# Kernel tuning notes

Measured on AMD Instinct MI355X. Metric: run time of the kernel, lower is better.

Reference implementation:

```python
import jax, jax.numpy as jnp
import numpy as np

DIM = 1024
HEADS = 16
HEAD_DIM = DIM // HEADS
HIDDEN = int(DIM * 4.0)
EPS = 1e-5


def setup_inputs() -> dict:
    key = jax.random.key(0)
    ks = jax.random.split(key, 16)
    s = 0.02
    inp = {
        'x': jax.random.normal(ks[0], (2, 2048, DIM), dtype=jnp.float32),
        'g1': jnp.ones((DIM,), jnp.float32),
        'b1': jnp.zeros((DIM,), jnp.float32),
        'Wq': jax.random.normal(ks[1], (DIM, DIM)) * s,
        'bq': jnp.zeros((DIM,), jnp.float32),
        'Wk': jax.random.normal(ks[2], (DIM, DIM)) * s,
        'bk': jnp.zeros((DIM,), jnp.float32),
        'Wv': jax.random.normal(ks[3], (DIM, DIM)) * s,
        'bv': jnp.zeros((DIM,), jnp.float32),
        'Wo': jax.random.normal(ks[4], (DIM, DIM)) * s,
        'bo': jnp.zeros((DIM,), jnp.float32),
        'g2': jnp.ones((DIM,), jnp.float32),
        'b2': jnp.zeros((DIM,), jnp.float32),
        'W1': jax.random.normal(ks[5], (DIM, HIDDEN)) * s,
        'bf1': jnp.zeros((HIDDEN,), jnp.float32),
        'W2': jax.random.normal(ks[6], (HIDDEN, DIM)) * s,
        'bf2': jnp.zeros((DIM,), jnp.float32),
    }
    return inp


def _layernorm(x, g, b):
    mu = jnp.mean(x, axis=-1, keepdims=True)
    var = jnp.mean((x - mu) ** 2, axis=-1, keepdims=True)
    return (x - mu) * jax.lax.rsqrt(var + EPS) * g + b


def _block(x, g1, b1, Wq, bq, Wk, bk, Wv, bv, Wo, bo, g2, b2, W1, bf1, W2, bf2):
    B, N, C = x.shape
    h = _layernorm(x, g1, b1)
    # project and split heads: [B, H, N, D]
    q = (h @ Wq + bq).reshape(B, N, HEADS, HEAD_DIM).transpose(0, 2, 1, 3)
    k = (h @ Wk + bk).reshape(B, N, HEADS, HEAD_DIM).transpose(0, 2, 1, 3)
    v = (h @ Wv + bv).reshape(B, N, HEADS, HEAD_DIM).transpose(0, 2, 1, 3)
    scale = HEAD_DIM ** -0.5
    attn = jnp.einsum('bhqd,bhkd->bhqk', q, k) * scale
    attn = jax.nn.softmax(attn, axis=-1)
    o = jnp.einsum('bhqk,bhkd->bhqd', attn, v)
    o = o.transpose(0, 2, 1, 3).reshape(B, N, C)
    x = x + (o @ Wo + bo)
    h = _layernorm(x, g2, b2)
    h = jax.nn.gelu(h @ W1 + bf1, approximate=False)
    x = x + (h @ W2 + bf2)
    return x


def reference(x, g1, b1, Wq, bq, Wk, bk, Wv, bv, Wo, bo, g2, b2, W1, bf1, W2, bf2):
    return _block(x, g1, b1, Wq, bq, Wk, bk, Wv, bv, Wo, bo, g2, b2, W1, bf1, W2, bf2)
```

## Files before the change

### kernel.cpp

```cpp
#include <hip/hip_runtime.h>
#include <hip/hip_bf16.h>
#include <math.h>


typedef unsigned short ushort_t;
typedef short short8 __attribute__((ext_vector_type(8)));
typedef float f32x4 __attribute__((ext_vector_type(4)));

#define TOKENS 4096
#define SEQ    2048
#define DIMC   1024
#define HID    4096

__device__ __forceinline__ float bf2f(ushort_t u) {
    union { float f; unsigned int u; } c; c.u = ((unsigned int)u) << 16; return c.f;
}
__device__ __forceinline__ ushort_t f2bf(float f) {
    union { float f; unsigned int u; } c; c.f = f;
    unsigned int u = c.u;
    unsigned int r = u + 0x7fffu + ((u >> 16) & 1u);
    return (ushort_t)(r >> 16);
}
__device__ __forceinline__ float gelu_f(float x) {
    const float y = 0.79788456080286536f * (x + 0.044715f * x * x * x);
    const float t = __expf(-2.0f * fabsf(y));
    const float th = (1.0f - t) / (1.0f + t);
    return 0.5f * x * (1.0f + copysignf(th, y));
}
__device__ __forceinline__ float load_elem(const void* p, size_t i, int isbf) {
    return isbf ? bf2f(((const ushort_t*)p)[i]) : ((const float*)p)[i];
}

__global__ __launch_bounds__(256) void detect_dtype(
    const ushort_t* __restrict__ x, int* __restrict__ flag)
{
    __shared__ int bad;
    if (threadIdx.x == 0) bad = 0;
    __syncthreads();
    for (int i = threadIdx.x; i < 4096; i += 256) {
        float v = bf2f(x[i]);
        if (!(fabsf(v) <= 1e6f)) bad = 1;
    }
    __syncthreads();
    if (threadIdx.x == 0) { flag[0] = (bad == 0) ? 1 : 0; flag[1] = 1; }
}

__global__ __launch_bounds__(256) void transpose_w_all(
    const void* __restrict__ Wq, const void* __restrict__ Wk,
    const void* __restrict__ Wv, const void* __restrict__ Wo,
    const void* __restrict__ W1, const void* __restrict__ W2,
    ushort_t* __restrict__ wsq, ushort_t* __restrict__ w1t,
    ushort_t* __restrict__ w2t, const int* __restrict__ flag)
{
    __shared__ ushort_t tile[32][33];
    const int isbf = *flag;
    const int id = blockIdx.x;
    const void* in; ushort_t* out; int K, N, bx, by;
    if (id < 4096) {
        const int z = id >> 10, t = id & 1023;
        in = z == 0 ? Wq : (z == 1 ? Wk : (z == 2 ? Wv : Wo));
        out = wsq + (size_t)z * DIMC * DIMC;
        K = DIMC; N = DIMC; bx = t & 31; by = t >> 5;
    } else if (id < 8192) {
        const int t = id - 4096;
        in = W1; out = w1t; K = DIMC; N = HID;
        bx = t & 127; by = t >> 7;
    } else {
        const int t = id - 8192;
        in = W2; out = w2t; K = HID; N = DIMC;
        bx = t & 31; by = t >> 5;
    }
    const int kb = by * 32, nb = bx * 32;
    const int tx = threadIdx.x & 31, ty = threadIdx.x >> 5;
    for (int i = 0; i < 4; i++) {
        int k = kb + ty + i * 8;
        tile[ty + i * 8][tx] = f2bf(load_elem(in, (size_t)k * N + nb + tx, isbf));
    }
    __syncthreads();
    for (int i = 0; i < 4; i++) {
        int n = nb + ty + i * 8;
        out[(size_t)n * K + kb + tx] = tile[tx][ty + i * 8];
    }
}

template<int INMODE>
__global__ __launch_bounds__(256) void ln_kernel(
    const void* __restrict__ in, const void* __restrict__ g,
    const void* __restrict__ b, const int* __restrict__ flag,
    ushort_t* __restrict__ out)
{
    const int isbf = *flag;
    const int t = blockIdx.x;
    const int tid = threadIdx.x;
    const size_t base = (size_t)t * DIMC;
    float v[4];
    for (int i = 0; i < 4; i++) {
        int idx = tid + i * 256;
        v[i] = (INMODE == 1) ? ((const float*)in)[base + idx]
                             : load_elem(in, base + idx, isbf);
    }
    float s  = v[0] + v[1] + v[2] + v[3];
    float s2 = v[0]*v[0] + v[1]*v[1] + v[2]*v[2] + v[3]*v[3];
    for (int off = 1; off < 64; off <<= 1) {
        s  += __shfl_xor(s,  off);
        s2 += __shfl_xor(s2, off);
    }
    __shared__ float red[8];
    const int wave = tid >> 6, lane = tid & 63;
    if (lane == 0) { red[wave] = s; red[wave + 4] = s2; }
    __syncthreads();
    s  = red[0] + red[1] + red[2] + red[3];
    s2 = red[4] + red[5] + red[6] + red[7];
    const float mu  = s * (1.0f / DIMC);
    const float var = s2 * (1.0f / DIMC) - mu * mu;
    const float inv = rsqrtf(fmaxf(var, 0.f) + 1e-5f);
    for (int i = 0; i < 4; i++) {
        int idx = tid + i * 256;
        float o = (v[i] - mu) * inv * load_elem(g, idx, isbf) + load_elem(b, idx, isbf);
        out[base + idx] = f2bf(o);
    }
}

template<int BN, int RES, int ACT, int OUTF>
__global__ __launch_bounds__(256) void gemm_bt(
    const ushort_t* __restrict__ A, const ushort_t* __restrict__ BT,
    const void* __restrict__ bias0, const void* __restrict__ bias1,
    const void* __restrict__ bias2, const void* __restrict__ resid,
    void* __restrict__ out0, void* __restrict__ out1, void* __restrict__ out2,
    int M, int N, int K, int Ksub, const int* __restrict__ flag)
{
    constexpr int BM   = 128;
    constexpr int JF   = BN / 32;
    constexpr int ASEG = BM / 16;
    constexpr int SPW  = (BM + BN) / 64;
    __shared__ __align__(16) ushort_t As[3][BM][32];
    __shared__ __align__(16) ushort_t Bs[3][BN][32];
    const int isbf = *flag;
    const int tid = threadIdx.x, lane = tid & 63, wave = tid >> 6;
    const int m0 = blockIdx.y * BM, n0 = blockIdx.x * BN;
    const int wm = (wave & 1) * 64;
    const int wn = (wave >> 1) * (BN / 2);
    const int lm = lane & 15, quad = lane >> 4;

    const void* biasp = bias0;
    void* outp = out0;
    int nout = N;
    int colmask = 0x7fffffff;
    int sel = 0;
    if (OUTF == 3) {
        sel = n0 >> 10;
        biasp = sel == 0 ? bias0 : (sel == 1 ? bias1 : bias2);
        outp  = sel == 0 ? out0  : (sel == 1 ? out1  : out2);
        nout = 1024; colmask = 1023;
    }
    int kbeg = 0;
    if (OUTF == 4) {
        kbeg = blockIdx.z * Ksub;
        outp = blockIdx.z ? out1 : out0;
    }

    f32x4 acc[4][JF];
    for (int i = 0; i < 4; i++)
        for (int j = 0; j < JF; j++)
            acc[i][j] = (f32x4){0.f, 0.f, 0.f, 0.f};

    const int lsw  = lane ^ ((lane >> 3) & 7);
    const int lrow = lsw >> 2;
    const int lcol = (lsw & 3) * 8;
    const int srd  = (4 * lm + quad);
    const int srz  = srd ^ ((srd >> 3) & 7);
    const int rsw  = srz >> 2;
    const int csw  = (srz & 3) * 8;

    const ushort_t* gpp[SPW];
    ushort_t* lpp[3][SPW];
#pragma unroll
    for (int s = 0; s < SPW; s++) {
        const int seg = wave * SPW + s;
        if (seg < ASEG) {
            gpp[s]    = &A[(size_t)(m0 + seg * 16 + lrow) * K + kbeg + lcol];
            lpp[0][s] = &As[0][seg * 16][0];
            lpp[1][s] = &As[1][seg * 16][0];
            lpp[2][s] = &As[2][seg * 16][0];
        } else {
            gpp[s]    = &BT[(size_t)(n0 + (seg - ASEG) * 16 + lrow) * K + kbeg + lcol];
            lpp[0][s] = &Bs[0][(seg - ASEG) * 16][0];
            lpp[1][s] = &Bs[1][(seg - ASEG) * 16][0];
            lpp[2][s] = &Bs[2][(seg - ASEG) * 16][0];
        }
    }

#define GEMM_STAGE(BUF, T)                                                    \
    {                                                                         \
        _Pragma("unroll")                                                     \
        for (int s = 0; s < SPW; s++)                                         \
            __builtin_amdgcn_global_load_lds(                                 \
                (const __attribute__((address_space(1))) unsigned int*)       \
                    (gpp[s] + (size_t)(T) * 32),                              \
                (__attribute__((address_space(3))) unsigned int*)lpp[BUF][s], \
                16, 0, 0);                                                    \
    }

#define GEMM_COMPUTE(BUF)                                                     \
    {                                                                         \
        short8 af[4], bfr[JF];                                                \
        _Pragma("unroll")                                                     \
        for (int i = 0; i < 4; i++)                                           \
            af[i] = *(const short8*)&As[BUF][wm + i * 16 + rsw][csw];         \
        _Pragma("unroll")                                                     \
        for (int j = 0; j < JF; j++)                                          \
            bfr[j] = *(const short8*)&Bs[BUF][wn + j * 16 + rsw][csw];        \
        _Pragma("unroll")                                                     \
        for (int i = 0; i < 4; i++)                                           \
            _Pragma("unroll")                                                 \
            for (int j = 0; j < JF; j++)                                      \
                acc[i][j] = __builtin_amdgcn_mfma_f32_16x16x32_bf16(          \
                    af[i], bfr[j], acc[i][j], 0, 0, 0);                       \
    }

#define GEMM_STEP(BC, BS, T)                                                  \
    if ((T) < nt) {                                                           \
        if ((T) + 1 < nt)                                                     \
            asm volatile("s_waitcnt vmcnt(3) lgkmcnt(0)" ::: "memory");       \
        else                                                                  \
            asm volatile("s_waitcnt vmcnt(0) lgkmcnt(0)" ::: "memory");       \
        __builtin_amdgcn_s_barrier();                                         \
        __builtin_amdgcn_sched_barrier(0);                                    \
        if ((T) + 2 < nt) GEMM_STAGE(BS, (T) + 2);                            \
        GEMM_COMPUTE(BC);                                                     \
    }

    const int nt = Ksub / 32;
    GEMM_STAGE(0, 0);
    GEMM_STAGE(1, 1);
    for (int t = 0; t < nt; t += 3) {
        GEMM_STEP(0, 2, t);
        GEMM_STEP(1, 0, t + 1);
        GEMM_STEP(2, 1, t + 2);
    }
#undef GEMM_STEP
#undef GEMM_STAGE
#undef GEMM_COMPUTE

    if (OUTF == 3 && sel == 2) {
        for (int j = 0; j < JF; j++) {
            const int colo = (n0 + wn + j * 16 + lm) & 1023;
            const float bv = load_elem(biasp, colo, isbf);
            for (int i = 0; i < 4; i++) {
                const int token = m0 + wm + i * 16 + quad * 4;
                const int bb = token >> 11, ss = token & 2047;
                unsigned int lo = (unsigned int)f2bf(acc[i][j][0] + bv)
                                | ((unsigned int)f2bf(acc[i][j][1] + bv) << 16);
                unsigned int hi = (unsigned int)f2bf(acc[i][j][2] + bv)
                                | ((unsigned int)f2bf(acc[i][j][3] + bv) << 16);
                *(uint2*)&((ushort_t*)outp)[(size_t)((bb << 10) + colo) * SEQ + ss] =
                    make_uint2(lo, hi);
            }
        }
        return;
    }

    for (int j = 0; j < JF; j++) {
        const int col  = n0 + wn + j * 16 + lm;
        const int colo = col & colmask;
        const float bv = (OUTF == 4) ? 0.f : load_elem(biasp, colo, isbf);
        for (int i = 0; i < 4; i++) {
            const int rbase = m0 + wm + i * 16 + quad * 4;
            for (int r = 0; r < 4; r++) {
                const size_t oi = (size_t)(rbase + r) * nout + colo;
                float v2 = acc[i][j][r] + bv;
                if (ACT == 1) v2 = gelu_f(v2);
                if (RES == 1) v2 += load_elem(resid, oi, isbf);
                if (RES == 2) v2 += ((const float*)resid)[oi];
                if (OUTF == 1 || OUTF == 4) { ((float*)outp)[oi] = v2; }
                else if (OUTF == 2) {
                    if (isbf) ((ushort_t*)outp)[oi] = f2bf(v2);
                    else      ((float*)outp)[oi] = v2;
                }
                else                { ((ushort_t*)outp)[oi] = f2bf(v2); }
            }
        }
    }
}

template<int RESRAW, int OUTF32>
__global__ __launch_bounds__(256) void splitk_reduce(
    const float* __restrict__ p0, const float* __restrict__ p1,
    const void* __restrict__ bias, const void* __restrict__ resid,
    void* __restrict__ out, const int* __restrict__ flag)
{
    const int isbf = *flag;
    const size_t i = ((size_t)blockIdx.x * 256 + threadIdx.x) * 4;
    const float4 a = *(const float4*)&p0[i];
    const float4 b = *(const float4*)&p1[i];
    const int col = (int)(i & 1023);
    float v[4] = {a.x + b.x, a.y + b.y, a.z + b.z, a.w + b.w};
    for (int c = 0; c < 4; c++) {
        v[c] += load_elem(bias, col + c, isbf);
        v[c] += RESRAW ? load_elem(resid, i + c, isbf) : ((const float*)resid)[i + c];
    }
    if (OUTF32) {
        *(float4*)&((float*)out)[i] = make_float4(v[0], v[1], v[2], v[3]);
    } else if (isbf) {
        unsigned int lo = (unsigned int)f2bf(v[0]) | ((unsigned int)f2bf(v[1]) << 16);
        unsigned int hi = (unsigned int)f2bf(v[2]) | ((unsigned int)f2bf(v[3]) << 16);
        *(uint2*)&((ushort_t*)out)[i] = make_uint2(lo, hi);
    } else {
        *(float4*)&((float*)out)[i] = make_float4(v[0], v[1], v[2], v[3]);
    }
}

__global__ __launch_bounds__(256) void attn_kernel(
    const ushort_t* __restrict__ q, const ushort_t* __restrict__ k,
    const ushort_t* __restrict__ vt, ushort_t* __restrict__ o)
{
    const int bh = blockIdx.x;
    const int b  = bh >> 4, h = bh & 15;
    const int q0 = blockIdx.y * 128;
    const int tid = threadIdx.x, lane = tid & 63, wave = tid >> 6;
    const int lm = lane & 15, quad = lane >> 4;

    __shared__ ushort_t Qs[128][72];
    __shared__ ushort_t Ks[64][72];
    __shared__ ushort_t Vt[64][72];
    __shared__ ushort_t Ps[4][32][72];

    const size_t base  = ((size_t)b * SEQ) * DIMC + h * 64;
    const size_t vbase = ((size_t)b * DIMC + h * 64) * SEQ;

    {
        const int er0 = (tid * 8) >> 6;
        const int ec0 = (tid * 8) & 63;
        for (int half = 0; half < 4; half++) {
            const int r = er0 + half * 32;
            short8 qq = *(const short8*)&q[base + (size_t)(q0 + r) * DIMC + ec0];
            short8 qs;
            for (int i = 0; i < 8; i++)
                qs[i] = (short)f2bf(bf2f((ushort_t)qq[i]) * 0.18033688011112042f);
            *(short8*)&Qs[r][ec0] = qs;
        }
    }
    __syncthreads();

    short8 qf[2][2];
    for (int qh = 0; qh < 2; qh++)
        for (int ks = 0; ks < 2; ks++)
            qf[qh][ks] = *(const short8*)&Qs[wave * 32 + qh * 16 + lm][quad * 8 + ks * 32];

    short8 onef;
    for (int i = 0; i < 8; i++) onef[i] = (short)0x3F80;

    f32x4 oacc[4][2], lacc[2];
    for (int j = 0; j < 4; j++)
        for (int qh = 0; qh < 2; qh++) oacc[j][qh] = (f32x4){0.f, 0.f, 0.f, 0.f};
    lacc[0] = (f32x4){0.f, 0.f, 0.f, 0.f};
    lacc[1] = (f32x4){0.f, 0.f, 0.f, 0.f};

    const int er = (tid * 8) >> 6;
    const int ec = (tid * 8) & 63;
    const int dd = tid >> 2;
    const int kg = tid & 3;

    short8 kreg0, kreg1, vreg0, vreg1;
    {
        kreg0 = *(const short8*)&k[base + (size_t)(er) * DIMC + ec];
        kreg1 = *(const short8*)&k[base + (size_t)(er + 32) * DIMC + ec];
        const size_t vsrc = vbase + (size_t)dd * SEQ + kg * 16;
        vreg0 = *(const short8*)&vt[vsrc];
        vreg1 = *(const short8*)&vt[vsrc + 8];
    }

    for (int kt = 0; kt < SEQ / 64; kt++) {
        __syncthreads();
        *(short8*)&Ks[er][ec]          = kreg0;
        *(short8*)&Ks[er + 32][ec]     = kreg1;
        *(short8*)&Vt[dd][kg * 16]     = vreg0;
        *(short8*)&Vt[dd][kg * 16 + 8] = vreg1;
        __syncthreads();
        if (kt + 1 < SEQ / 64) {
            const int kn = (kt + 1) * 64;
            kreg0 = *(const short8*)&k[base + (size_t)(kn + er) * DIMC + ec];
            kreg1 = *(const short8*)&k[base + (size_t)(kn + er + 32) * DIMC + ec];
            const size_t vsrc = vbase + (size_t)dd * SEQ + kn + kg * 16;
            vreg0 = *(const short8*)&vt[vsrc];
            vreg1 = *(const short8*)&vt[vsrc + 8];
        }

        f32x4 st[4][2];
        for (int j = 0; j < 4; j++)
            for (int qh = 0; qh < 2; qh++) st[j][qh] = (f32x4){0.f, 0.f, 0.f, 0.f};
        for (int ks = 0; ks < 2; ks++) {
            for (int j = 0; j < 4; j++) {
                short8 kf = *(const short8*)&Ks[j * 16 + lm][quad * 8 + ks * 32];
                for (int qh = 0; qh < 2; qh++)
                    st[j][qh] = __builtin_amdgcn_mfma_f32_16x16x32_bf16(kf, qf[qh][ks], st[j][qh], 0, 0, 0);
            }
        }

        for (int j = 0; j < 4; j++)
            for (int qh = 0; qh < 2; qh++) {
                unsigned int u0 = __float_as_uint(__builtin_amdgcn_exp2f(st[j][qh][0]));
                unsigned int u1 = __float_as_uint(__builtin_amdgcn_exp2f(st[j][qh][1]));
                unsigned int u2 = __float_as_uint(__builtin_amdgcn_exp2f(st[j][qh][2]));
                unsigned int u3 = __float_as_uint(__builtin_amdgcn_exp2f(st[j][qh][3]));
                unsigned int lo = (u1 & 0xffff0000u) | (u0 >> 16);
                unsigned int hi = (u3 & 0xffff0000u) | (u2 >> 16);
                *(uint2*)&Ps[wave][qh * 16 + lm][j * 16 + quad * 4] = make_uint2(lo, hi);
            }

        for (int ks = 0; ks < 2; ks++) {
            for (int qh = 0; qh < 2; qh++) {
                short8 pf = *(const short8*)&Ps[wave][qh * 16 + lm][quad * 8 + ks * 32];
                lacc[qh] = __builtin_amdgcn_mfma_f32_16x16x32_bf16(pf, onef, lacc[qh], 0, 0, 0);
                for (int j = 0; j < 4; j++) {
                    short8 vf = *(const short8*)&Vt[j * 16 + lm][quad * 8 + ks * 32];
                    oacc[j][qh] = __builtin_amdgcn_mfma_f32_16x16x32_bf16(pf, vf, oacc[j][qh], 0, 0, 0);
                }
            }
        }
    }

    float rinv[2][4];
    for (int qh = 0; qh < 2; qh++)
        for (int r = 0; r < 4; r++) rinv[qh][r] = 1.0f / fmaxf(lacc[qh][r], 1e-30f);

    for (int j = 0; j < 4; j++)
        for (int qh = 0; qh < 2; qh++)
            for (int r = 0; r < 4; r++) {
                const int row = q0 + wave * 32 + qh * 16 + quad * 4 + r;
                o[base + (size_t)row * DIMC + j * 16 + lm] = f2bf(oacc[j][qh][r] * rinv[qh][r]);
            }
}

extern "C" void kernel_launch(void* const* d_in, const int* in_sizes, int n_in,
                              void* d_out, int out_size, void* d_ws, size_t ws_size,
                              hipStream_t stream)
{
    const void* x   = d_in[0];
    const void* g1  = d_in[1];
    const void* b1  = d_in[2];
    const void* Wq  = d_in[3];
    const void* bq  = d_in[4];
    const void* Wk  = d_in[5];
    const void* bk  = d_in[6];
    const void* Wv  = d_in[7];
    const void* bv  = d_in[8];
    const void* Wo  = d_in[9];
    const void* bo  = d_in[10];
    const void* g2  = d_in[11];
    const void* b2  = d_in[12];
    const void* W1  = d_in[13];
    const void* bf1 = d_in[14];
    const void* W2  = d_in[15];
    const void* bf2 = d_in[16];

    const size_t SZ_TOKD_BF = (size_t)TOKENS * DIMC * 2;
    const size_t SZ_TOKD_F  = (size_t)TOKENS * DIMC * 4;
    const size_t SZ_W_SQ    = (size_t)DIMC * DIMC * 2;
    const size_t SZ_W_FF    = (size_t)DIMC * HID * 2;
    const size_t SZ_FF1     = (size_t)TOKENS * HID * 2;

    char* ws = (char*)d_ws;
    size_t off = 0;
    int*      flag = (int*)(ws + off);       off += 256;
    ushort_t* h    = (ushort_t*)(ws + off);  off += SZ_TOKD_BF;
    ushort_t* qb   = (ushort_t*)(ws + off);  off += SZ_TOKD_BF;
    ushort_t* kb_  = (ushort_t*)(ws + off);  off += SZ_TOKD_BF;
    ushort_t* ao   = (ushort_t*)(ws + off);  off += SZ_TOKD_BF;
    ushort_t* vtg  = (ushort_t*)(ws + off);  off += SZ_TOKD_BF;
    float*    x1f  = (float*)qb;
    float*    pa   = (float*)qb;
    float*    p0   = (float*)ao;
    ushort_t* wqt  = (ushort_t*)(ws + off);  off += SZ_W_SQ;
    ushort_t* wkt  = (ushort_t*)(ws + off);  off += SZ_W_SQ;
    ushort_t* wvt  = (ushort_t*)(ws + off);  off += SZ_W_SQ;
    ushort_t* wot  = (ushort_t*)(ws + off);  off += SZ_W_SQ;
    ushort_t* w1t  = (ushort_t*)(ws + off);  off += SZ_W_FF;
    ushort_t* w2t  = (ushort_t*)(ws + off);  off += SZ_W_FF;
    ushort_t* ff1  = (ushort_t*)(ws + off);  off += SZ_FF1;
    float*    p1   = (float*)(ws + off);     off += SZ_TOKD_F;
    if (ws_size < off) return;

    (void)wkt; (void)wvt;

    detect_dtype<<<1, 256, 0, stream>>>((const ushort_t*)x, flag);

    transpose_w_all<<<12288, 256, 0, stream>>>(Wq, Wk, Wv, Wo, W1, W2,
                                               wqt, w1t, w2t, flag);

    ln_kernel<0><<<TOKENS, 256, 0, stream>>>(x, g1, b1, flag, h);

    gemm_bt<64, 0, 0, 3><<<dim3(48, 32), 256, 0, stream>>>(
        h, wqt, bq, bk, bv, nullptr, qb, kb_, vtg, TOKENS, 3072, DIMC, DIMC, flag);

    attn_kernel<<<dim3(32, 16), 256, 0, stream>>>(qb, kb_, vtg, ao);

    gemm_bt<64, 0, 0, 4><<<dim3(16, 32, 2), 256, 0, stream>>>(
        ao, wot, nullptr, nullptr, nullptr, nullptr, pa, p1, nullptr,
        TOKENS, DIMC, DIMC, DIMC / 2, flag);

    splitk_reduce<1, 1><<<TOKENS * DIMC / 1024, 256, 0, stream>>>(
        pa, p1, bo, x, x1f, flag);

    ln_kernel<1><<<TOKENS, 256, 0, stream>>>(x1f, g2, b2, flag, h);

    gemm_bt<64, 0, 1, 0><<<dim3(64, 32), 256, 0, stream>>>(
        h, w1t, bf1, nullptr, nullptr, nullptr, ff1, nullptr, nullptr,
        TOKENS, HID, DIMC, DIMC, flag);

    gemm_bt<64, 0, 0, 4><<<dim3(16, 32, 2), 256, 0, stream>>>(
        ff1, w2t, nullptr, nullptr, nullptr, nullptr, p0, p1, nullptr,
        TOKENS, DIMC, HID, HID / 2, flag);

    splitk_reduce<0, 0><<<TOKENS * DIMC / 1024, 256, 0, stream>>>(
        p0, p1, bf2, x1f, d_out, flag);
}
```

Before: 414.1 us.

## Fuse split-K reduce with LayerNorm, widen FFN1 tile, double-buffer QKV GEMM

Adds a reduce_ln kernel that sums the split-K partials, adds bias and residual, writes x1f and computes the second LayerNorm in one pass, replacing two launches and a round trip of x1f. The FFN1 GEMM moves to a 128-wide N tile, which gives more reuse per block and half as many blocks. The QKV GEMM switches to a new two-buffer pipeline that uses plain __syncthreads, trading load/compute overlap for lower LDS use. With BN=128, SPW becomes 4, so the wait count is adjusted to vmcnt(4).

```diff
diff --git a/kernel.cpp b/kernel.cpp
--- a/kernel.cpp
+++ b/kernel.cpp
@@ -121,7 +121,55 @@
     }
 }
 
-template<int BN, int RES, int ACT, int OUTF>
+__global__ __launch_bounds__(256) void reduce_ln(
+    const float* __restrict__ p0, const float* __restrict__ p1,
+    const void* __restrict__ bias, const void* __restrict__ resid,
+    float* __restrict__ x1f, const void* __restrict__ g,
+    const void* __restrict__ b, const int* __restrict__ flag,
+    ushort_t* __restrict__ out)
+{
+    const int isbf = *flag;
+    const int t = blockIdx.x;
+    const int tid = threadIdx.x;
+    const size_t base = (size_t)t * DIMC;
+    const int col = tid * 4;
+    const size_t i = base + col;
+    const float4 a  = *(const float4*)&p0[i];
+    const float4 bb = *(const float4*)&p1[i];
+    float v[4] = {a.x + bb.x, a.y + bb.y, a.z + bb.z, a.w + bb.w};
+    for (int c = 0; c < 4; c++) {
+        v[c] += load_elem(bias, col + c, isbf);
+        v[c] += load_elem(resid, i + c, isbf);
+    }
+    *(float4*)&x1f[i] = make_float4(v[0], v[1], v[2], v[3]);
+
+    float s  = v[0] + v[1] + v[2] + v[3];
+    float s2 = v[0]*v[0] + v[1]*v[1] + v[2]*v[2] + v[3]*v[3];
+    for (int off = 1; off < 64; off <<= 1) {
+        s  += __shfl_xor(s,  off);
+        s2 += __shfl_xor(s2, off);
+    }
+    __shared__ float red[8];
+    const int wave = tid >> 6, lane = tid & 63;
+    if (lane == 0) { red[wave] = s; red[wave + 4] = s2; }
+    __syncthreads();
+    s  = red[0] + red[1] + red[2] + red[3];
+    s2 = red[4] + red[5] + red[6] + red[7];
+    const float mu  = s * (1.0f / DIMC);
+    const float var = s2 * (1.0f / DIMC) - mu * mu;
+    const float inv = rsqrtf(fmaxf(var, 0.f) + 1e-5f);
+    ushort_t ob[4];
+    for (int c = 0; c < 4; c++) {
+        float o = (v[c] - mu) * inv * load_elem(g, col + c, isbf)
+                + load_elem(b, col + c, isbf);
+        ob[c] = f2bf(o);
+    }
+    unsigned int lo = (unsigned int)ob[0] | ((unsigned int)ob[1] << 16);
+    unsigned int hi = (unsigned int)ob[2] | ((unsigned int)ob[3] << 16);
+    *(uint2*)&out[i] = make_uint2(lo, hi);
+}
+
+template<int BN, int RES, int ACT, int OUTF, int NBUF>
 __global__ __launch_bounds__(256) void gemm_bt(
     const ushort_t* __restrict__ A, const ushort_t* __restrict__ BT,
     const void* __restrict__ bias0, const void* __restrict__ bias1,
@@ -133,8 +181,8 @@
     constexpr int JF   = BN / 32;
     constexpr int ASEG = BM / 16;
     constexpr int SPW  = (BM + BN) / 64;
-    __shared__ __align__(16) ushort_t As[3][BM][32];
-    __shared__ __align__(16) ushort_t Bs[3][BN][32];
+    __shared__ __align__(16) ushort_t As[NBUF][BM][32];
+    __shared__ __align__(16) ushort_t Bs[NBUF][BN][32];
     const int isbf = *flag;
     const int tid = threadIdx.x, lane = tid & 63, wave = tid >> 6;
     const int m0 = blockIdx.y * BM, n0 = blockIdx.x * BN;
@@ -173,20 +221,18 @@
     const int csw  = (srz & 3) * 8;
 
     const ushort_t* gpp[SPW];
-    ushort_t* lpp[3][SPW];
+    ushort_t* lpp[NBUF][SPW];
 #pragma unroll
     for (int s = 0; s < SPW; s++) {
         const int seg = wave * SPW + s;
         if (seg < ASEG) {
-            gpp[s]    = &A[(size_t)(m0 + seg * 16 + lrow) * K + kbeg + lcol];
-            lpp[0][s] = &As[0][seg * 16][0];
-            lpp[1][s] = &As[1][seg * 16][0];
-            lpp[2][s] = &As[2][seg * 16][0];
+            gpp[s] = &A[(size_t)(m0 + seg * 16 + lrow) * K + kbeg + lcol];
+#pragma unroll
+            for (int bfi = 0; bfi < NBUF; bfi++) lpp[bfi][s] = &As[bfi][seg * 16][0];
         } else {
-            gpp[s]    = &BT[(size_t)(n0 + (seg - ASEG) * 16 + lrow) * K + kbeg + lcol];
-            lpp[0][s] = &Bs[0][(seg - ASEG) * 16][0];
-            lpp[1][s] = &Bs[1][(seg - ASEG) * 16][0];
-            lpp[2][s] = &Bs[2][(seg - ASEG) * 16][0];
+            gpp[s] = &BT[(size_t)(n0 + (seg - ASEG) * 16 + lrow) * K + kbeg + lcol];
+#pragma unroll
+            for (int bfi = 0; bfi < NBUF; bfi++) lpp[bfi][s] = &Bs[bfi][(seg - ASEG) * 16][0];
         }
     }
 
@@ -220,10 +266,14 @@
 
 #define GEMM_STEP(BC, BS, T)                                                  \
     if ((T) < nt) {                                                           \
-        if ((T) + 1 < nt)                                                     \
-            asm volatile("s_waitcnt vmcnt(3) lgkmcnt(0)" ::: "memory");       \
-        else                                                                  \
+        if ((T) + 1 < nt) {                                                   \
+            if constexpr (SPW == 3)                                           \
+                asm volatile("s_waitcnt vmcnt(3) lgkmcnt(0)" ::: "memory");   \
+            else                                                              \
+                asm volatile("s_waitcnt vmcnt(4) lgkmcnt(0)" ::: "memory");   \
+        } else {                                                              \
             asm volatile("s_waitcnt vmcnt(0) lgkmcnt(0)" ::: "memory");       \
+        }                                                                     \
         __builtin_amdgcn_s_barrier();                                         \
         __builtin_amdgcn_sched_barrier(0);                                    \
         if ((T) + 2 < nt) GEMM_STAGE(BS, (T) + 2);                            \
@@ -231,12 +281,25 @@
     }
 
     const int nt = Ksub / 32;
-    GEMM_STAGE(0, 0);
-    GEMM_STAGE(1, 1);
-    for (int t = 0; t < nt; t += 3) {
-        GEMM_STEP(0, 2, t);
-        GEMM_STEP(1, 0, t + 1);
-        GEMM_STEP(2, 1, t + 2);
+    if constexpr (NBUF == 3) {
+        GEMM_STAGE(0, 0);
+        GEMM_STAGE(1, 1);
+        for (int t = 0; t < nt; t += 3) {
+            GEMM_STEP(0, 2, t);
+            GEMM_STEP(1, 0, t + 1);
+            GEMM_STEP(2, 1, t + 2);
+        }
+    } else {
+        GEMM_STAGE(0, 0);
+        __syncthreads();
+        for (int t = 0; t < nt; t += 2) {
+            GEMM_STAGE(1, t + 1);
+            GEMM_COMPUTE(0);
+            __syncthreads();
+            if (t + 2 < nt) GEMM_STAGE(0, t + 2);
+            GEMM_COMPUTE(1);
+            __syncthreads();
+        }
     }
 #undef GEMM_STEP
 #undef GEMM_STAGE
@@ -490,25 +553,23 @@
 
     ln_kernel<0><<<TOKENS, 256, 0, stream>>>(x, g1, b1, flag, h);
 
-    gemm_bt<64, 0, 0, 3><<<dim3(48, 32), 256, 0, stream>>>(
+    gemm_bt<64, 0, 0, 3, 2><<<dim3(48, 32), 256, 0, stream>>>(
         h, wqt, bq, bk, bv, nullptr, qb, kb_, vtg, TOKENS, 3072, DIMC, DIMC, flag);
 
     attn_kernel<<<dim3(32, 16), 256, 0, stream>>>(qb, kb_, vtg, ao);
 
-    gemm_bt<64, 0, 0, 4><<<dim3(16, 32, 2), 256, 0, stream>>>(
+    gemm_bt<64, 0, 0, 4, 3><<<dim3(16, 32, 2), 256, 0, stream>>>(
         ao, wot, nullptr, nullptr, nullptr, nullptr, pa, p1, nullptr,
         TOKENS, DIMC, DIMC, DIMC / 2, flag);
 
-    splitk_reduce<1, 1><<<TOKENS * DIMC / 1024, 256, 0, stream>>>(
-        pa, p1, bo, x, x1f, flag);
-
-    ln_kernel<1><<<TOKENS, 256, 0, stream>>>(x1f, g2, b2, flag, h);
-
-    gemm_bt<64, 0, 1, 0><<<dim3(64, 32), 256, 0, stream>>>(
+    reduce_ln<<<TOKENS, 256, 0, stream>>>(
+        pa, p1, bo, x, x1f, g2, b2, flag, h);
+
+    gemm_bt<128, 0, 1, 0, 3><<<dim3(32, 32), 256, 0, stream>>>(
         h, w1t, bf1, nullptr, nullptr, nullptr, ff1, nullptr, nullptr,
         TOKENS, HID, DIMC, DIMC, flag);
 
-    gemm_bt<64, 0, 0, 4><<<dim3(16, 32, 2), 256, 0, stream>>>(
+    gemm_bt<64, 0, 0, 4, 3><<<dim3(16, 32, 2), 256, 0, stream>>>(
         ff1, w2t, nullptr, nullptr, nullptr, nullptr, p0, p1, nullptr,
         TOKENS, DIMC, HID, HID / 2, flag);
 
```

Result: no change. 408.0 us (-1.5%).
